# Optimization experiments

Hardware: AMD Instinct MI355X
Metric: run time of the kernel (lower is better)

## Reference

```python
import jax, jax.numpy as jnp
import numpy as np

EMB_SIZE = 256
NUM_EMBS = 8192


def setup_inputs() -> dict:
    key = jax.random.key(0)
    k1, k2 = jax.random.split(key)
    x = jax.random.normal(k1, (32, EMB_SIZE, 32, 32), dtype=jnp.float32)
    # matches torch init: uniform_(-1/num_embs, 1/num_embs)
    codebook = jax.random.uniform(
        k2, (NUM_EMBS, EMB_SIZE), dtype=jnp.float32,
        minval=-1.0 / NUM_EMBS, maxval=1.0 / NUM_EMBS)
    return {"x": x, "codebook": codebook}


def reference(x, codebook):
    b, c, h, w = x.shape
    # [b,c,h,w] -> [b*h*w, c]
    xf = jnp.transpose(x, (0, 2, 3, 1)).reshape(b * h * w, c)
    # squared euclidean distances; argmin identical to argmin of cdist
    x_sq = jnp.sum(xf * xf, axis=1, keepdims=True)            # [N,1]
    cb_sq = jnp.sum(codebook * codebook, axis=1)              # [K]
    cross = jnp.einsum('nc,kc->nk', xf, codebook)             # [N,K]
    d2 = x_sq - 2.0 * cross + cb_sq[None, :]
    indices = jnp.argmin(d2, axis=1)                          # [N] int
    quantized = codebook[indices]                             # [N,c] gather
    quantized = quantized.reshape(b, h, w, c).transpose(0, 3, 1, 2)
    return quantized, indices
```

## Files before the change

kernel.cpp:

```cpp
#include <hip/hip_runtime.h>
#include <hip/hip_bf16.h>

#define C_   256
#define P_   1024
#define N_   32768
#define K_   8192
#define QOFF 8388608
#define CAP  64
#define EPS  1e-3f

#define XBF_OFF   0u
#define CBBF_OFF  16777216u
#define CAND_OFF  20971520u
#define CNT_OFF   29360128u
#define GMIN_OFF  29491200u
#define CBSQ_OFF  29622272u
#define XSQ_OFF   29655040u

typedef __attribute__((ext_vector_type(8))) short bf16x8;
typedef __attribute__((ext_vector_type(4))) float f32x4;

__device__ inline unsigned fkey(float f) {
    unsigned u = __float_as_uint(f);
    return (u & 0x80000000u) ? ~u : (u | 0x80000000u);
}
__device__ inline float funkey(unsigned k) {
    unsigned u = (k & 0x80000000u) ? (k ^ 0x80000000u) : ~k;
    return __uint_as_float(u);
}
__device__ inline void gload_lds16(const void* g, void* l) {
    __builtin_amdgcn_global_load_lds((const __attribute__((address_space(1))) void*)g,
                                     (__attribute__((address_space(3))) void*)l, 16, 0, 0);
}
__device__ inline unsigned short bfbits(float f) {
    __hip_bfloat16 h = __float2bfloat16(f);
    return *(unsigned short*)&h;
}

__global__ __launch_bounds__(256) void prep_x(const float* __restrict__ x,
                                              char* __restrict__ outb) {
    __shared__ float xs[C_][66];
    unsigned short* xbf = (unsigned short*)(outb + XBF_OFF);
    float*    xsq  = (float*)(outb + XSQ_OFF);
    int*      cnt  = (int*)(outb + CNT_OFF);
    unsigned* gmin = (unsigned*)(outb + GMIN_OFF);
    const int t = threadIdx.x;
    const int n0 = blockIdx.x * 64;
    const int b = n0 >> 10, p0 = n0 & 1023;
    for (int i = 0; i < 64; ++i) {
        int f = t + 256 * i; int c = f >> 6, nl = f & 63;
        xs[c][nl] = x[(b * C_ + c) * P_ + p0 + nl];
    }
    __syncthreads();
    if (t < 64) {
        double acc = 0.0;
        for (int c = 0; c < C_; ++c) { float v = xs[c][t]; float pq = v * v; acc += (double)pq; }
        xsq[n0 + t] = (float)acc;
        cnt[n0 + t] = 0;
        gmin[n0 + t] = 0xFFFFFFFFu;
    }
    for (int i = 0; i < 64; ++i) {
        int f = t + 256 * i; int nl = f >> 8, c = f & 255;
        xbf[(n0 + nl) * C_ + c] = bfbits(xs[c][nl]);
    }
}

__global__ __launch_bounds__(256) void prep_cb(const float* __restrict__ cb,
                                               char* __restrict__ outb) {
    float* cbsq = (float*)(outb + CBSQ_OFF);
    unsigned short* cbbf = (unsigned short*)(outb + CBBF_OFF);
    const int row  = blockIdx.x * 4 + (threadIdx.x >> 6);
    const int lane = threadIdx.x & 63;
    const float4 v = *reinterpret_cast<const float4*>(cb + row * C_ + lane * 4);
    float p0 = v.x * v.x, p1 = v.y * v.y, p2 = v.z * v.z, p3 = v.w * v.w;
    double acc = (double)p0 + (double)p1 + (double)p2 + (double)p3;
    for (int off = 32; off; off >>= 1) acc += __shfl_down(acc, off, 64);
    if (lane == 0) cbsq[row] = (float)acc;
    ushort4 u = { bfbits(v.x), bfbits(v.y), bfbits(v.z), bfbits(v.w) };
    *reinterpret_cast<ushort4*>(cbbf + row * C_ + lane * 4) = u;
}

template <int COLLECT>
__global__ __launch_bounds__(256) void vq_mfma(char* __restrict__ outb) {
    __shared__ unsigned short tA[128 * 64];
    __shared__ unsigned short tB[128 * 64];
    __shared__ float cbsq_l[128];
    __shared__ float th_l[128];
    const unsigned short* xbf  = (const unsigned short*)(outb + XBF_OFF);
    const unsigned short* cbbf = (const unsigned short*)(outb + CBBF_OFF);
    const float* cbsq = (const float*)(outb + CBSQ_OFF);
    unsigned* gmin = (unsigned*)(outb + GMIN_OFF);
    int* cnt  = (int*)(outb + CNT_OFF);
    int* cand = (int*)(outb + CAND_OFF);

    const int t = threadIdx.x;
    const int l = t & 63, w = t >> 6;
    const int wn = w >> 1, wk = w & 1;
    const int n0 = blockIdx.x * 128;
    const int k0 = COLLECT ? blockIdx.y * 128 : blockIdx.y * 256;

    if (t < 128) {
        cbsq_l[t] = cbsq[k0 + t];
        th_l[t] = COLLECT ? (funkey(gmin[n0 + t]) + EPS) : 0.f;
    }

    f32x4 acc[4][4];
    #pragma unroll
    for (int i = 0; i < 4; ++i)
        #pragma unroll
        for (int j = 0; j < 4; ++j) acc[i][j] = (f32x4)(0.f);

    const int lr = l >> 3;
    const int lc = (l & 7) * 8;

    for (int ct = 0; ct < 4; ++ct) {
        const int c0 = ct * 64;
        #pragma unroll
        for (int s = 0; s < 4; ++s) {
            const int row = w * 8 + s * 32 + lr;
            gload_lds16(xbf  + (unsigned)(n0 + row) * C_ + c0 + lc, (char*)tA + w * 1024 + s * 4096);
            gload_lds16(cbbf + (unsigned)(k0 + row) * C_ + c0 + lc, (char*)tB + w * 1024 + s * 4096);
        }
        __syncthreads();
        #pragma unroll
        for (int cs = 0; cs < 2; ++cs) {
            bf16x8 a[4], bb[4];
            const int gb = (cs * 4 + (l >> 4)) * 16;
            #pragma unroll
            for (int i = 0; i < 4; ++i) {
                const int rowA = wn * 64 + i * 16 + (l & 15);
                a[i]  = *reinterpret_cast<const bf16x8*>((const char*)tA + rowA * 128 + gb);
                const int rowB = wk * 64 + i * 16 + (l & 15);
                bb[i] = *reinterpret_cast<const bf16x8*>((const char*)tB + rowB * 128 + gb);
            }
            #pragma unroll
            for (int i = 0; i < 4; ++i)
                #pragma unroll
                for (int j = 0; j < 4; ++j)
                    acc[i][j] = __builtin_amdgcn_mfma_f32_16x16x32_bf16(a[i], bb[j], acc[i][j], 0, 0, 0);
        }
        __syncthreads();
    }

    if (COLLECT) {
        #pragma unroll
        for (int i = 0; i < 4; ++i) {
            float th[4];
            #pragma unroll
            for (int q = 0; q < 4; ++q) th[q] = th_l[wn * 64 + i * 16 + (l >> 4) * 4 + q];
            #pragma unroll
            for (int j = 0; j < 4; ++j) {
                const float cq = cbsq_l[wk * 64 + j * 16 + (l & 15)];
                const int   kg = k0 + wk * 64 + j * 16 + (l & 15);
                #pragma unroll
                for (int q = 0; q < 4; ++q) {
                    const float s = fmaf(-2.0f, acc[i][j][q], cq);
                    if (s < th[q]) {
                        const int ng = n0 + wn * 64 + i * 16 + (l >> 4) * 4 + q;
                        const int pos = atomicAdd(&cnt[ng], 1);
                        if (pos < CAP) cand[ng * CAP + pos] = kg;
                    }
                }
            }
        }
    } else {
        #pragma unroll
        for (int i = 0; i < 4; ++i) {
            float m[4] = {3e38f, 3e38f, 3e38f, 3e38f};
            #pragma unroll
            for (int j = 0; j < 4; ++j) {
                const float cq = cbsq_l[wk * 64 + j * 16 + (l & 15)];
                #pragma unroll
                for (int q = 0; q < 4; ++q)
                    m[q] = fminf(m[q], fmaf(-2.0f, acc[i][j][q], cq));
            }
            #pragma unroll
            for (int q = 0; q < 4; ++q) {
                #pragma unroll
                for (int off = 1; off < 16; off <<= 1)
                    m[q] = fminf(m[q], __shfl_xor(m[q], off, 64));
                if ((l & 15) == 0)
                    atomicMin(&gmin[n0 + wn * 64 + i * 16 + (l >> 4) * 4 + q], fkey(m[q]));
            }
        }
    }
}

__global__ __launch_bounds__(256) void rescore(const float* __restrict__ x,
                                               const float* __restrict__ cb,
                                               float* __restrict__ outf,
                                               char* __restrict__ outb) {
    __shared__ float xrow[4][C_];
    const float* cbsq = (const float*)(outb + CBSQ_OFF);
    const float* xsq  = (const float*)(outb + XSQ_OFF);
    const int*   cnt  = (const int*)(outb + CNT_OFF);
    const int*   cand = (const int*)(outb + CAND_OFF);
    const int t = threadIdx.x, l = t & 63, w = t >> 6;
    const int n = blockIdx.x * 4 + w;
    const int b = n >> 10, p = n & 1023;
    #pragma unroll
    for (int i = 0; i < 4; ++i) {
        const int c = l + i * 64;
        xrow[w][c] = x[(b * C_ + c) * P_ + p];
    }
    __syncthreads();
    int m = cnt[n]; if (m > CAP) m = CAP;
    float s2 = 3e38f; int bk = 0x7FFFFFFF;
    if (l < m) {
        const int k = cand[n * CAP + l];
        float acc = 0.f;
        const float4* cb4 = reinterpret_cast<const float4*>(cb + k * C_);
        #pragma unroll 4
        for (int c4 = 0; c4 < 64; ++c4) {
            const float4 cv = cb4[c4];
            acc = fmaf(xrow[w][c4 * 4 + 0], cv.x, acc);
            acc = fmaf(xrow[w][c4 * 4 + 1], cv.y, acc);
            acc = fmaf(xrow[w][c4 * 4 + 2], cv.z, acc);
            acc = fmaf(xrow[w][c4 * 4 + 3], cv.w, acc);
        }
        const float s1 = xsq[n] - 2.0f * acc;
        s2 = s1 + cbsq[k];
        bk = k;
    }
    #pragma unroll
    for (int off = 32; off; off >>= 1) {
        const float so = __shfl_xor(s2, off, 64);
        const int   ko = __shfl_xor(bk, off, 64);
        if (so < s2 || (so == s2 && ko < bk)) { s2 = so; bk = ko; }
    }
    if (l == 0) outf[QOFF + n] = (float)bk;
}

__global__ __launch_bounds__(256) void gather(const float* __restrict__ cb,
                                              float* __restrict__ outf) {
    __shared__ int kf[64];
    const int t = threadIdx.x;
    const int n0 = blockIdx.x * 64;
    const int b = n0 >> 10, p0 = n0 & 1023;
    if (t < 64) kf[t] = (int)outf[QOFF + n0 + t];
    __syncthreads();
    for (int i = 0; i < 64; ++i) {
        int f = t + 256 * i; int c = f >> 6, nl = f & 63;
        outf[(b * C_ + c) * P_ + p0 + nl] = cb[kf[nl] * C_ + c];
    }
}

extern "C" void kernel_launch(void* const* d_in, const int* in_sizes, int n_in,
                              void* d_out, int out_size, void* d_ws, size_t ws_size,
                              hipStream_t stream) {
    const float* x  = (const float*)d_in[0];
    const float* cb = (const float*)d_in[1];
    float* outf = (float*)d_out;
    char*  outb = (char*)d_out;

    prep_x<<<N_ / 64, 256, 0, stream>>>(x, outb);
    prep_cb<<<K_ / 4, 256, 0, stream>>>(cb, outb);
    vq_mfma<0><<<dim3(N_ / 128, 32), 256, 0, stream>>>(outb);
    vq_mfma<1><<<dim3(N_ / 128, 64), 256, 0, stream>>>(outb);
    rescore<<<N_ / 4, 256, 0, stream>>>(x, cb, outf, outb);
    gather<<<N_ / 64, 256, 0, stream>>>(cb, outf);
}
```

Baseline: 517.1 us.

## Fuse two-pass min/collect GEMMs into single online-threshold pass with LDS swizzle

Replaces the separate global-min GEMM pass and the candidate-collection GEMM pass with one kernel that walks a K chunk per block, keeps a running per-row minimum in LDS, and collects candidates against that running threshold. This halves the bf16 GEMM work and removes the global atomicMin round trip, but the early running threshold is loose, so more candidates are collected; CAP is raised and rescore now loops over more than 64 candidates. It also XOR-swizzles the LDS tile layout to reduce bank conflicts. The grid drops to 256x2 blocks, which lowers parallelism and may leave compute units idle.

```diff
diff --git a/kernel.cpp b/kernel.cpp
--- a/kernel.cpp
+++ b/kernel.cpp
@@ -6,28 +6,21 @@
 #define N_   32768
 #define K_   8192
 #define QOFF 8388608
-#define CAP  64
-#define EPS  1e-3f
+#define CAP  88
+#define EPS  8e-4f
+#define KSPLIT 2
+#define KCHUNK (K_ / KSPLIT)
 
 #define XBF_OFF   0u
 #define CBBF_OFF  16777216u
 #define CAND_OFF  20971520u
-#define CNT_OFF   29360128u
-#define GMIN_OFF  29491200u
-#define CBSQ_OFF  29622272u
-#define XSQ_OFF   29655040u
+#define CNT_OFF   32505856u
+#define XSQ_OFF   32636928u
+#define CBSQ_OFF  32768000u
 
 typedef __attribute__((ext_vector_type(8))) short bf16x8;
 typedef __attribute__((ext_vector_type(4))) float f32x4;
 
-__device__ inline unsigned fkey(float f) {
-    unsigned u = __float_as_uint(f);
-    return (u & 0x80000000u) ? ~u : (u | 0x80000000u);
-}
-__device__ inline float funkey(unsigned k) {
-    unsigned u = (k & 0x80000000u) ? (k ^ 0x80000000u) : ~k;
-    return __uint_as_float(u);
-}
 __device__ inline void gload_lds16(const void* g, void* l) {
     __builtin_amdgcn_global_load_lds((const __attribute__((address_space(1))) void*)g,
                                      (__attribute__((address_space(3))) void*)l, 16, 0, 0);
@@ -41,9 +34,8 @@
                                               char* __restrict__ outb) {
     __shared__ float xs[C_][66];
     unsigned short* xbf = (unsigned short*)(outb + XBF_OFF);
-    float*    xsq  = (float*)(outb + XSQ_OFF);
-    int*      cnt  = (int*)(outb + CNT_OFF);
-    unsigned* gmin = (unsigned*)(outb + GMIN_OFF);
+    float* xsq = (float*)(outb + XSQ_OFF);
+    int*   cnt = (int*)(outb + CNT_OFF);
     const int t = threadIdx.x;
     const int n0 = blockIdx.x * 64;
     const int b = n0 >> 10, p0 = n0 & 1023;
@@ -57,7 +49,6 @@
         for (int c = 0; c < C_; ++c) { float v = xs[c][t]; float pq = v * v; acc += (double)pq; }
         xsq[n0 + t] = (float)acc;
         cnt[n0 + t] = 0;
-        gmin[n0 + t] = 0xFFFFFFFFu;
     }
     for (int i = 0; i < 64; ++i) {
         int f = t + 256 * i; int nl = f >> 8, c = f & 255;
@@ -80,16 +71,15 @@
     *reinterpret_cast<ushort4*>(cbbf + row * C_ + lane * 4) = u;
 }
 
-template <int COLLECT>
-__global__ __launch_bounds__(256) void vq_mfma(char* __restrict__ outb) {
+__global__ __launch_bounds__(256) void vq_online(char* __restrict__ outb) {
     __shared__ unsigned short tA[128 * 64];
     __shared__ unsigned short tB[128 * 64];
-    __shared__ float cbsq_l[128];
-    __shared__ float th_l[128];
+    __shared__ float csq_l[KCHUNK];
+    __shared__ float thbuf[128];
+    __shared__ float wmin[2][128];
     const unsigned short* xbf  = (const unsigned short*)(outb + XBF_OFF);
     const unsigned short* cbbf = (const unsigned short*)(outb + CBBF_OFF);
     const float* cbsq = (const float*)(outb + CBSQ_OFF);
-    unsigned* gmin = (unsigned*)(outb + GMIN_OFF);
     int* cnt  = (int*)(outb + CNT_OFF);
     int* cand = (int*)(outb + CAND_OFF);
 
@@ -97,90 +87,97 @@
     const int l = t & 63, w = t >> 6;
     const int wn = w >> 1, wk = w & 1;
     const int n0 = blockIdx.x * 128;
-    const int k0 = COLLECT ? blockIdx.y * 128 : blockIdx.y * 256;
-
-    if (t < 128) {
-        cbsq_l[t] = cbsq[k0 + t];
-        th_l[t] = COLLECT ? (funkey(gmin[n0 + t]) + EPS) : 0.f;
-    }
-
-    f32x4 acc[4][4];
+    const int chunk0 = blockIdx.y * KCHUNK;
+
     #pragma unroll
     for (int i = 0; i < 4; ++i)
-        #pragma unroll
-        for (int j = 0; j < 4; ++j) acc[i][j] = (f32x4)(0.f);
-
-    const int lr = l >> 3;
-    const int lc = (l & 7) * 8;
-
-    for (int ct = 0; ct < 4; ++ct) {
-        const int c0 = ct * 64;
-        #pragma unroll
-        for (int s = 0; s < 4; ++s) {
-            const int row = w * 8 + s * 32 + lr;
-            gload_lds16(xbf  + (unsigned)(n0 + row) * C_ + c0 + lc, (char*)tA + w * 1024 + s * 4096);
-            gload_lds16(cbbf + (unsigned)(k0 + row) * C_ + c0 + lc, (char*)tB + w * 1024 + s * 4096);
+        gload_lds16(cbsq + chunk0 + i * 1024 + w * 256 + l * 4,
+                    (char*)csq_l + i * 4096 + w * 1024);
+    if (t < 128) thbuf[t] = 3.0e38f;
+
+    const int lr3 = l >> 3;
+    const int lg  = ((l & 7) ^ (lr3 & 7)) * 8;
+
+    for (int p = 0; p < KCHUNK / 128; ++p) {
+        const int k0 = chunk0 + p * 128;
+
+        f32x4 acc[4][4];
+        #pragma unroll
+        for (int i = 0; i < 4; ++i)
+            #pragma unroll
+            for (int j = 0; j < 4; ++j) acc[i][j] = (f32x4)(0.f);
+
+        for (int ct = 0; ct < 4; ++ct) {
+            const int c0 = ct * 64;
+            #pragma unroll
+            for (int s = 0; s < 4; ++s) {
+                const int row = w * 8 + s * 32 + lr3;
+                gload_lds16(xbf  + (unsigned)(n0 + row) * C_ + c0 + lg, (char*)tA + w * 1024 + s * 4096);
+                gload_lds16(cbbf + (unsigned)(k0 + row) * C_ + c0 + lg, (char*)tB + w * 1024 + s * 4096);
+            }
+            __syncthreads();
+            #pragma unroll
+            for (int cs = 0; cs < 2; ++cs) {
+                const int gb = (((cs * 4) + (l >> 4)) ^ (l & 7)) * 16;
+                bf16x8 a[4], bb[4];
+                #pragma unroll
+                for (int i = 0; i < 4; ++i) {
+                    a[i]  = *reinterpret_cast<const bf16x8*>((const char*)tA + (wn * 64 + i * 16 + (l & 15)) * 128 + gb);
+                    bb[i] = *reinterpret_cast<const bf16x8*>((const char*)tB + (wk * 64 + i * 16 + (l & 15)) * 128 + gb);
+                }
+                #pragma unroll
+                for (int i = 0; i < 4; ++i)
+                    #pragma unroll
+                    for (int j = 0; j < 4; ++j)
+                        acc[i][j] = __builtin_amdgcn_mfma_f32_16x16x32_bf16(a[i], bb[j], acc[i][j], 0, 0, 0);
+            }
+            __syncthreads();
+        }
+
+        float cq[4];
+        #pragma unroll
+        for (int j = 0; j < 4; ++j) cq[j] = csq_l[p * 128 + wk * 64 + j * 16 + (l & 15)];
+
+        float mrow[4][4];
+        #pragma unroll
+        for (int i = 0; i < 4; ++i)
+            #pragma unroll
+            for (int q = 0; q < 4; ++q) {
+                float m = fmaf(-2.0f, acc[i][0][q], cq[0]);
+                #pragma unroll
+                for (int j = 1; j < 4; ++j) m = fminf(m, fmaf(-2.0f, acc[i][j][q], cq[j]));
+                #pragma unroll
+                for (int off = 1; off < 16; off <<= 1) m = fminf(m, __shfl_xor(m, off, 64));
+                mrow[i][q] = m;
+            }
+        if ((l & 15) == 0) {
+            #pragma unroll
+            for (int i = 0; i < 4; ++i)
+                #pragma unroll
+                for (int q = 0; q < 4; ++q)
+                    wmin[wk][wn * 64 + i * 16 + (l >> 4) * 4 + q] = mrow[i][q];
         }
         __syncthreads();
-        #pragma unroll
-        for (int cs = 0; cs < 2; ++cs) {
-            bf16x8 a[4], bb[4];
-            const int gb = (cs * 4 + (l >> 4)) * 16;
-            #pragma unroll
-            for (int i = 0; i < 4; ++i) {
-                const int rowA = wn * 64 + i * 16 + (l & 15);
-                a[i]  = *reinterpret_cast<const bf16x8*>((const char*)tA + rowA * 128 + gb);
-                const int rowB = wk * 64 + i * 16 + (l & 15);
-                bb[i] = *reinterpret_cast<const bf16x8*>((const char*)tB + rowB * 128 + gb);
-            }
-            #pragma unroll
-            for (int i = 0; i < 4; ++i)
-                #pragma unroll
-                for (int j = 0; j < 4; ++j)
-                    acc[i][j] = __builtin_amdgcn_mfma_f32_16x16x32_bf16(a[i], bb[j], acc[i][j], 0, 0, 0);
-        }
+        if (t < 128) thbuf[t] = fminf(thbuf[t], fminf(wmin[0][t], wmin[1][t]));
         __syncthreads();
-    }
-
-    if (COLLECT) {
+
         #pragma unroll
         for (int i = 0; i < 4; ++i) {
             float th[4];
             #pragma unroll
-            for (int q = 0; q < 4; ++q) th[q] = th_l[wn * 64 + i * 16 + (l >> 4) * 4 + q];
+            for (int q = 0; q < 4; ++q) th[q] = thbuf[wn * 64 + i * 16 + (l >> 4) * 4 + q] + EPS;
             #pragma unroll
             for (int j = 0; j < 4; ++j) {
-                const float cq = cbsq_l[wk * 64 + j * 16 + (l & 15)];
-                const int   kg = k0 + wk * 64 + j * 16 + (l & 15);
+                const int kg = k0 + wk * 64 + j * 16 + (l & 15);
                 #pragma unroll
                 for (int q = 0; q < 4; ++q) {
-                    const float s = fmaf(-2.0f, acc[i][j][q], cq);
+                    const float s = fmaf(-2.0f, acc[i][j][q], cq[j]);
                     if (s < th[q]) {
                         const int ng = n0 + wn * 64 + i * 16 + (l >> 4) * 4 + q;
                         const int pos = atomicAdd(&cnt[ng], 1);
                         if (pos < CAP) cand[ng * CAP + pos] = kg;
                     }
                 }
-            }
-        }
-    } else {
-        #pragma unroll
-        for (int i = 0; i < 4; ++i) {
-            float m[4] = {3e38f, 3e38f, 3e38f, 3e38f};
-            #pragma unroll
-            for (int j = 0; j < 4; ++j) {
-                const float cq = cbsq_l[wk * 64 + j * 16 + (l & 15)];
-                #pragma unroll
-                for (int q = 0; q < 4; ++q)
-                    m[q] = fminf(m[q], fmaf(-2.0f, acc[i][j][q], cq));
-            }
-            #pragma unroll
-            for (int q = 0; q < 4; ++q) {
-                #pragma unroll
-                for (int off = 1; off < 16; off <<= 1)
-                    m[q] = fminf(m[q], __shfl_xor(m[q], off, 64));
-                if ((l & 15) == 0)
-                    atomicMin(&gmin[n0 + wn * 64 + i * 16 + (l >> 4) * 4 + q], fkey(m[q]));
             }
         }
     }
@@ -206,8 +203,8 @@
     __syncthreads();
     int m = cnt[n]; if (m > CAP) m = CAP;
     float s2 = 3e38f; int bk = 0x7FFFFFFF;
-    if (l < m) {
-        const int k = cand[n * CAP + l];
+    for (int cidx = l; cidx < m; cidx += 64) {
+        const int k = cand[n * CAP + cidx];
         float acc = 0.f;
         const float4* cb4 = reinterpret_cast<const float4*>(cb + k * C_);
         #pragma unroll 4
@@ -219,8 +216,8 @@
             acc = fmaf(xrow[w][c4 * 4 + 3], cv.w, acc);
         }
         const float s1 = xsq[n] - 2.0f * acc;
-        s2 = s1 + cbsq[k];
-        bk = k;
+        const float sc = s1 + cbsq[k];
+        if (sc < s2 || (sc == s2 && k < bk)) { s2 = sc; bk = k; }
     }
     #pragma unroll
     for (int off = 32; off; off >>= 1) {
@@ -255,8 +252,7 @@
 
     prep_x<<<N_ / 64, 256, 0, stream>>>(x, outb);
     prep_cb<<<K_ / 4, 256, 0, stream>>>(cb, outb);
-    vq_mfma<0><<<dim3(N_ / 128, 32), 256, 0, stream>>>(outb);
-    vq_mfma<1><<<dim3(N_ / 128, 64), 256, 0, stream>>>(outb);
+    vq_online<<<dim3(N_ / 128, KSPLIT), 256, 0, stream>>>(outb);
     rescore<<<N_ / 4, 256, 0, stream>>>(x, cb, outf, outb);
     gather<<<N_ / 64, 256, 0, stream>>>(cb, outf);
 }
```

New measurement: 872.2 us. 68.7% more time.
